# Performance work log

Measured on AMD Instinct MI355X. Metric: run time of the kernel, lower is better.

The kernel has to match this reference:

```python
import jax, jax.numpy as jnp
from jax import lax
import numpy as np

NUM_BINS = 16
EPS = 1e-8


def setup_inputs() -> dict:
    key = jax.random.key(0)
    x = jax.random.normal(key, (32, 512, 4096), dtype=jnp.float32)
    return {"x": x}


def reference(x):
    B, C, L = x.shape  # [B, C, L]
    nb = NUM_BINS
    # g = mean over sequence -> [B, C]
    g = x.mean(axis=2)
    # cosine similarity along channel dim between each column x[:, :, l] and g
    dot = jnp.einsum('bcl,bc->bl', x, g)                      # [B, L]
    xn = jnp.sqrt(jnp.sum(x * x, axis=1))                     # [B, L]
    gn = jnp.sqrt(jnp.sum(g * g, axis=1, keepdims=True))      # [B, 1]
    cos = dot / jnp.maximum(xn * gn, EPS)                     # [B, L]
    S = cos.reshape(-1)                                       # [B*L]
    # torch.linspace on tensor endpoints detaches -> stop_gradient for fidelity
    min_S = lax.stop_gradient(S.min())
    max_S = lax.stop_gradient(S.max())
    levels = min_S + jnp.arange(nb, dtype=S.dtype) * (max_S - min_S) / (nb - 1)  # [nb]
    # soft triangular binning: (1 - |S - L_n|) inside a half-width 0.5/nb window
    d = jnp.abs(S[:, None] - levels[None, :])                 # [B*L, nb]
    E = jnp.where(d < 0.5 / nb, 1.0 - d, 0.0)
    E = E.reshape(B, L, nb)
    count_map = E.sum(axis=1)                                 # [B, nb]
    count_map = count_map / count_map.sum(axis=1, keepdims=True)
    # adaptive_avg_pool1d from length 1 to C//nb just replicates the value
    out = jnp.broadcast_to(count_map[:, :, None], (B, nb, C // nb))
    return out
```

## Files before the change

### kernel.cpp

```cpp
#include <hip/hip_runtime.h>

typedef float f4 __attribute__((ext_vector_type(4)));

#define BB 32
#define CC 512
#define LL 4096
#define NB 16
#define EPSF 1e-8f

__global__ __launch_bounds__(256, 2)
void k_main(const float* __restrict__ x, float* __restrict__ g,
            f4* __restrict__ pd4, f4* __restrict__ ps4) {
    __shared__ float lds[4 * LL];
    __shared__ float sgv[4];
    const int tid = threadIdx.x;
    const int w = tid >> 6, lane = tid & 63;
    const int b  = blockIdx.x >> 4;
    const int c0 = (blockIdx.x & 15) * 32;
    const f4* xr = (const f4*)(x + ((size_t)b * CC + c0 + w) * LL);

    f4 d4[4], s4[4];
#pragma unroll
    for (int j = 0; j < 4; ++j) { d4[j] = (f4)0.f; s4[j] = (f4)0.f; }

    f4 v[16];
#pragma unroll
    for (int i = 0; i < 16; ++i) v[i] = __builtin_nontemporal_load(&xr[i * 64 + lane]);

    for (int st = 0; st < 8; ++st) {
        float s = 0.f;
#pragma unroll
        for (int i = 0; i < 16; ++i) s += (v[i][0] + v[i][1]) + (v[i][2] + v[i][3]);
#pragma unroll
        for (int off = 32; off; off >>= 1) s += __shfl_down(s, off, 64);
        __syncthreads();
        if (lane == 0) {
            float gv = s * (1.0f / LL);
            sgv[w] = gv;
            g[b * CC + c0 + st * 4 + w] = gv;
        }
        f4* lrow = (f4*)&lds[w * LL];
#pragma unroll
        for (int i = 0; i < 16; ++i) lrow[i * 64 + lane] = v[i];
        __syncthreads();
        if (st < 7) {
            const f4* nxt = xr + (size_t)(st + 1) * 4096;
#pragma unroll
            for (int i = 0; i < 16; ++i) v[i] = __builtin_nontemporal_load(&nxt[i * 64 + lane]);
        }
#pragma unroll
        for (int c = 0; c < 4; ++c) {
            const float gv = sgv[c];
            const f4* lc4 = (const f4*)&lds[c * LL];
#pragma unroll
            for (int j = 0; j < 4; ++j) {
                f4 f = lc4[j * 256 + tid];
#pragma unroll
                for (int k = 0; k < 4; ++k) {
                    d4[j][k] = fmaf(f[k], gv, d4[j][k]);
                    s4[j][k] = fmaf(f[k], f[k], s4[j][k]);
                }
            }
        }
    }
#pragma unroll
    for (int j = 0; j < 4; ++j) {
        pd4[(size_t)blockIdx.x * 1024 + j * 256 + tid] = d4[j];
        ps4[(size_t)blockIdx.x * 1024 + j * 256 + tid] = s4[j];
    }
}

__global__ void k_reduce(const float* __restrict__ g,
                         const f4* __restrict__ pd4, const f4* __restrict__ ps4,
                         f4* __restrict__ cosv4,
                         float* __restrict__ pmin, float* __restrict__ pmax) {
    const int tid = threadIdx.x;
    const int w = tid >> 6, lane = tid & 63;
    const int b = blockIdx.x >> 3;
    const int q = blockIdx.x & 7;
    const int s = q * 128 + tid;

    f4 g4 = ((const f4*)g)[b * 128 + tid];
    float sq = fmaf(g4[0], g4[0], fmaf(g4[1], g4[1], fmaf(g4[2], g4[2], g4[3] * g4[3])));
#pragma unroll
    for (int off = 32; off; off >>= 1) sq += __shfl_down(sq, off, 64);
    __shared__ float sw[2];
    if (lane == 0) sw[w] = sq;
    __syncthreads();
    const float gn = sqrtf(sw[0] + sw[1]);

    f4 pdv = (f4)0.f, psv = (f4)0.f;
#pragma unroll
    for (int ch = 0; ch < 16; ++ch) {
        pdv += pd4[(((size_t)b * 16 + ch) << 10) + s];
        psv += ps4[(((size_t)b * 16 + ch) << 10) + s];
    }
    f4 cs;
#pragma unroll
    for (int k = 0; k < 4; ++k)
        cs[k] = pdv[k] / fmaxf(sqrtf(psv[k]) * gn, EPSF);
    cosv4[(size_t)b * 1024 + s] = cs;

    float mn = fminf(fminf(cs[0], cs[1]), fminf(cs[2], cs[3]));
    float mx = fmaxf(fmaxf(cs[0], cs[1]), fmaxf(cs[2], cs[3]));
#pragma unroll
    for (int off = 32; off; off >>= 1) {
        mn = fminf(mn, __shfl_down(mn, off, 64));
        mx = fmaxf(mx, __shfl_down(mx, off, 64));
    }
    __shared__ float smn[2], smx[2];
    if (lane == 0) { smn[w] = mn; smx[w] = mx; }
    __syncthreads();
    if (tid == 0) {
        pmin[blockIdx.x] = fminf(smn[0], smn[1]);
        pmax[blockIdx.x] = fmaxf(smx[0], smx[1]);
    }
}

__global__ void k_hist(const float* __restrict__ cosv,
                       const float* __restrict__ pmin, const float* __restrict__ pmax,
                       float* __restrict__ out) {
    const int b = blockIdx.x;
    const int wave = threadIdx.x >> 6, lane = threadIdx.x & 63;

    float mn = pmin[threadIdx.x];
    float mx = pmax[threadIdx.x];
#pragma unroll
    for (int off = 32; off; off >>= 1) {
        mn = fminf(mn, __shfl_down(mn, off, 64));
        mx = fmaxf(mx, __shfl_down(mx, off, 64));
    }
    __shared__ float smn[4], smx[4];
    if (lane == 0) { smn[wave] = mn; smx[wave] = mx; }
    __syncthreads();
    mn = fminf(fminf(smn[0], smn[1]), fminf(smn[2], smn[3]));
    mx = fmaxf(fmaxf(smx[0], smx[1]), fmaxf(smx[2], smx[3]));
    const float range = mx - mn;

    float bins[NB];
#pragma unroll
    for (int n = 0; n < NB; ++n) bins[n] = 0.f;

    const float* cb = cosv + (b << 12);
    for (int l = threadIdx.x; l < LL; l += 256) {
        float s = cb[l];
#pragma unroll
        for (int n = 0; n < NB; ++n) {
            float lev = mn + ((float)n * range) / 15.0f;
            float d = fabsf(s - lev);
            bins[n] += (d < 0.03125f) ? (1.0f - d) : 0.f;
        }
    }
#pragma unroll
    for (int n = 0; n < NB; ++n) {
#pragma unroll
        for (int off = 32; off; off >>= 1) bins[n] += __shfl_down(bins[n], off, 64);
    }
    __shared__ float sb[4][NB];
    if (lane == 0) {
#pragma unroll
        for (int n = 0; n < NB; ++n) sb[wave][n] = bins[n];
    }
    __syncthreads();
    __shared__ float colsum[NB];
    if (threadIdx.x < NB) {
        const int n = threadIdx.x;
        colsum[n] = sb[0][n] + sb[1][n] + sb[2][n] + sb[3][n];
    }
    __syncthreads();
    float total = 0.f;
#pragma unroll
    for (int n = 0; n < NB; ++n) total += colsum[n];
    {
        const int i0 = threadIdx.x;
        out[b * (NB * 32) + i0]       = colsum[i0 >> 5] / total;
        out[b * (NB * 32) + i0 + 256] = colsum[(i0 + 256) >> 5] / total;
    }
}

extern "C" void kernel_launch(void* const* d_in, const int* in_sizes, int n_in,
                              void* d_out, int out_size, void* d_ws, size_t ws_size,
                              hipStream_t stream) {
    const float* x = (const float*)d_in[0];
    float* out = (float*)d_out;
    float* ws  = (float*)d_ws;

    float* g    = ws;
    float* cosv = ws + 16384;
    float* pmin = ws + 16384 + 131072;
    float* pmax = pmin + 256;
    f4*    pd4  = (f4*)(pmax + 256);
    f4*    ps4  = pd4 + 524288;

    k_main<<<512, 256, 0, stream>>>(x, g, pd4, ps4);
    k_reduce<<<256, 128, 0, stream>>>(g, pd4, ps4, (f4*)cosv, pmin, pmax);
    k_hist<<<32, 256, 0, stream>>>(cosv, pmin, pmax, out);
}
```

Before: 68.08 us.

## Give each wave its own channels and accumulate in registers, reducing once via LDS

```diff
diff --git a/kernel.cpp b/kernel.cpp
--- a/kernel.cpp
+++ b/kernel.cpp
@@ -11,62 +11,54 @@
 __global__ __launch_bounds__(256, 2)
 void k_main(const float* __restrict__ x, float* __restrict__ g,
             f4* __restrict__ pd4, f4* __restrict__ ps4) {
-    __shared__ float lds[4 * LL];
-    __shared__ float sgv[4];
+    __shared__ f4 ldsD[1024], ldsS[1024];
     const int tid = threadIdx.x;
     const int w = tid >> 6, lane = tid & 63;
     const int b  = blockIdx.x >> 4;
     const int c0 = (blockIdx.x & 15) * 32;
-    const f4* xr = (const f4*)(x + ((size_t)b * CC + c0 + w) * LL);
 
-    f4 d4[4], s4[4];
+    f4 dA[16], sA[16];
 #pragma unroll
-    for (int j = 0; j < 4; ++j) { d4[j] = (f4)0.f; s4[j] = (f4)0.f; }
+    for (int i = 0; i < 16; ++i) { dA[i] = (f4)0.f; sA[i] = (f4)0.f; }
 
-    f4 v[16];
+    const f4* base = (const f4*)(x + ((size_t)b * CC + c0 + w * 8) * LL);
+    for (int cc = 0; cc < 8; ++cc) {
+        const f4* row = base + (size_t)cc * 1024;
+        f4 v[16];
 #pragma unroll
-    for (int i = 0; i < 16; ++i) v[i] = __builtin_nontemporal_load(&xr[i * 64 + lane]);
-
-    for (int st = 0; st < 8; ++st) {
+        for (int i = 0; i < 16; ++i) v[i] = __builtin_nontemporal_load(&row[i * 64 + lane]);
         float s = 0.f;
 #pragma unroll
         for (int i = 0; i < 16; ++i) s += (v[i][0] + v[i][1]) + (v[i][2] + v[i][3]);
 #pragma unroll
         for (int off = 32; off; off >>= 1) s += __shfl_down(s, off, 64);
-        __syncthreads();
-        if (lane == 0) {
-            float gv = s * (1.0f / LL);
-            sgv[w] = gv;
-            g[b * CC + c0 + st * 4 + w] = gv;
-        }
-        f4* lrow = (f4*)&lds[w * LL];
+        s = __shfl(s, 0, 64);
+        const float gv = s * (1.0f / LL);
+        if (lane == 0) g[b * CC + c0 + w * 8 + cc] = gv;
 #pragma unroll
-        for (int i = 0; i < 16; ++i) lrow[i * 64 + lane] = v[i];
-        __syncthreads();
-        if (st < 7) {
-            const f4* nxt = xr + (size_t)(st + 1) * 4096;
+        for (int i = 0; i < 16; ++i) {
 #pragma unroll
-            for (int i = 0; i < 16; ++i) v[i] = __builtin_nontemporal_load(&nxt[i * 64 + lane]);
-        }
-#pragma unroll
-        for (int c = 0; c < 4; ++c) {
-            const float gv = sgv[c];
-            const f4* lc4 = (const f4*)&lds[c * LL];
-#pragma unroll
-            for (int j = 0; j < 4; ++j) {
-                f4 f = lc4[j * 256 + tid];
-#pragma unroll
-                for (int k = 0; k < 4; ++k) {
-                    d4[j][k] = fmaf(f[k], gv, d4[j][k]);
-                    s4[j][k] = fmaf(f[k], f[k], s4[j][k]);
-                }
+            for (int k = 0; k < 4; ++k) {
+                dA[i][k] = fmaf(v[i][k], gv, dA[i][k]);
+                sA[i][k] = fmaf(v[i][k], v[i][k], sA[i][k]);
             }
         }
     }
+    for (int ww = 0; ww < 4; ++ww) {
+        if (w == ww) {
+#pragma unroll
+            for (int i = 0; i < 16; ++i) {
+                const int idx = i * 64 + lane;
+                if (ww == 0) { ldsD[idx] = dA[i];  ldsS[idx] = sA[i]; }
+                else         { ldsD[idx] += dA[i]; ldsS[idx] += sA[i]; }
+            }
+        }
+        __syncthreads();
+    }
 #pragma unroll
     for (int j = 0; j < 4; ++j) {
-        pd4[(size_t)blockIdx.x * 1024 + j * 256 + tid] = d4[j];
-        ps4[(size_t)blockIdx.x * 1024 + j * 256 + tid] = s4[j];
+        pd4[(size_t)blockIdx.x * 1024 + j * 256 + tid] = ldsD[j * 256 + tid];
+        ps4[(size_t)blockIdx.x * 1024 + j * 256 + tid] = ldsS[j * 256 + tid];
     }
 }
 
```

After: 69.50 us. 2.1% more time.
